# Kernel optimization log

Measured on AMD Instinct MI355X. Metric: run time of the kernel, lower is better.

## Reference

```python
import jax, jax.numpy as jnp
import numpy as np

NUM_ROI = 400
N_GRAPHS = 128
N_NODES = NUM_ROI * N_GRAPHS            # 51200
N_EDGES = N_NODES * 40                  # 2048000
EMB = [128, 128]
BN_EPS = 1e-5


def mish(x):
    return x * jnp.tanh(jax.nn.softplus(x))


def gcn_conv(x, row, col, ew, W, b, n_nodes):
    """PyG GCNConv: h = XW; add self-loops (w=1); sym-normalize; scatter-add; + bias."""
    h = x @ W                                            # [N, out]
    loops = jnp.arange(n_nodes, dtype=row.dtype)
    row_ = jnp.concatenate([row, loops])
    col_ = jnp.concatenate([col, loops])
    ew_ = jnp.concatenate([ew, jnp.ones((n_nodes,), ew.dtype)])
    deg = jax.ops.segment_sum(ew_, col_, num_segments=n_nodes)
    dinv = jnp.where(deg > 0, jax.lax.rsqrt(deg), 0.0)
    norm = dinv[row_] * ew_ * dinv[col_]                 # [E+N]
    msg = norm[:, None] * h[row_]                        # gather + scale
    out = jax.ops.segment_sum(msg, col_, num_segments=n_nodes)
    return out + b


def setup_inputs() -> dict:
    key = jax.random.key(0)
    ks = jax.random.split(key, 16)
    inp = {
        "x": jax.random.normal(ks[0], (N_NODES, NUM_ROI), jnp.float32),
        "edge_index": jax.random.randint(ks[1], (2, N_EDGES), 0, N_NODES, jnp.int64)
        if jax.config.jax_enable_x64 else jax.random.randint(ks[1], (2, N_EDGES), 0, N_NODES, jnp.int32),
        "edge_attr": jax.random.uniform(ks[2], (N_EDGES,), jnp.float32),
        "batch": jnp.repeat(jnp.arange(N_GRAPHS), NUM_ROI),
        "conv1_w": jax.random.normal(ks[3], (NUM_ROI, EMB[0]), jnp.float32) * 0.05,
        "conv1_b": jax.random.normal(ks[4], (EMB[0],), jnp.float32) * 0.05,
        "conv2_w": jax.random.normal(ks[5], (EMB[0], EMB[1]), jnp.float32) * 0.05,
        "conv2_b": jax.random.normal(ks[6], (EMB[1],), jnp.float32) * 0.05,
        "ro_w": jax.random.normal(ks[7], (EMB[1], 8), jnp.float32) * 0.05,
        "ro_b": jax.random.normal(ks[8], (8,), jnp.float32) * 0.05,
        "fc1_w": jax.random.normal(ks[9], (8 * NUM_ROI, NUM_ROI), jnp.float32) * 0.02,
        "fc1_b": jax.random.normal(ks[10], (NUM_ROI,), jnp.float32) * 0.02,
        "bn_gamma": jnp.ones((NUM_ROI,), jnp.float32),
        "bn_beta": jnp.zeros((NUM_ROI,), jnp.float32),
        "fc2_w": jax.random.normal(ks[11], (NUM_ROI, 2), jnp.float32) * 0.05,
        "fc2_b": jax.random.normal(ks[12], (2,), jnp.float32) * 0.05,
    }
    return inp


def reference(x, edge_index, edge_attr, batch,
              conv1_w, conv1_b, conv2_w, conv2_b,
              ro_w, ro_b, fc1_w, fc1_b, bn_gamma, bn_beta, fc2_w, fc2_b):
    n = x.shape[0]
    row, col = edge_index[0], edge_index[1]
    h = mish(gcn_conv(x, row, col, edge_attr, conv1_w, conv1_b, n))
    h = mish(gcn_conv(h, row, col, edge_attr, conv2_w, conv2_b, n))
    out = mish(h @ ro_w + ro_b)                          # [N, 8]
    feats = out.reshape(-1, NUM_ROI * 8)                 # [B, 3200]
    z = feats @ fc1_w + fc1_b                            # [B, 400]
    # BatchNorm1d (training mode: batch statistics, biased variance)
    mu = jnp.mean(z, axis=0)
    var = jnp.mean((z - mu) ** 2, axis=0)
    zn = (z - mu) * jax.lax.rsqrt(var + BN_EPS) * bn_gamma + bn_beta
    logits = mish(zn) @ fc2_w + fc2_b                    # [B, 2]
    return logits
```

## Files before the change

### kernel.cpp

```cpp
#include <hip/hip_runtime.h>
#include <hip/hip_fp16.h>
#include <math.h>

#define NN 51200
#define NE 2048000
#define F 128
#define NB 1000
#define EPB 2048
#define NBKT 200

typedef _Float16 half8 __attribute__((ext_vector_type(8)));
typedef float floatx4 __attribute__((ext_vector_type(4)));

__device__ __forceinline__ float mish_f(float x) {
  if (x > 20.0f) return x;
  float e = __expf(x);
  float w = 1.0f + e;
  w = w * w;
  return x * (w - 1.0f) / (w + 1.0f);
}

__global__ __launch_bounds__(256) void k_chist(const int* __restrict__ ei, unsigned* __restrict__ G) {
  __shared__ unsigned hist[NBKT];
  int blk = blockIdx.x, t = threadIdx.x;
  for (int i = t; i < NBKT; i += 256) hist[i] = 0u;
  __syncthreads();
  int base = blk * EPB;
  for (int it = 0; it < EPB; it += 256) {
    int dst = ei[NE + base + it + t];
    atomicAdd(&hist[dst >> 8], 1u);
  }
  __syncthreads();
  for (int i = t; i < NBKT; i += 256) G[(size_t)i * NB + blk] = hist[i];
}

__global__ __launch_bounds__(64) void k_bscan(unsigned* __restrict__ G, unsigned* __restrict__ btot) {
  int b = blockIdx.x, l = threadIdx.x;
  unsigned base = (unsigned)l * 16;
  unsigned loc[16];
  unsigned s = 0;
#pragma unroll
  for (int i = 0; i < 16; ++i) {
    unsigned idx = base + i;
    unsigned x = (idx < NB) ? G[(size_t)b * NB + idx] : 0u;
    loc[i] = s;
    s += x;
  }
  unsigned run = s;
#pragma unroll
  for (int off = 1; off < 64; off <<= 1) {
    unsigned y = __shfl_up(run, off);
    if (l >= off) run += y;
  }
  unsigned excl = run - s;
#pragma unroll
  for (int i = 0; i < 16; ++i) {
    unsigned idx = base + i;
    if (idx < NB) G[(size_t)b * NB + idx] = excl + loc[i];
  }
  if (l == 63) btot[b] = run;
}

__global__ __launch_bounds__(256) void k_bbase(const unsigned* __restrict__ btot, unsigned* __restrict__ bbase) {
  int t = threadIdx.x, lane = t & 63, wid = t >> 6;
  unsigned v = (t < NBKT) ? btot[t] : 0u;
  unsigned x = v;
#pragma unroll
  for (int off = 1; off < 64; off <<= 1) {
    unsigned y = __shfl_up(x, off);
    if (lane >= off) x += y;
  }
  __shared__ unsigned ws4[4];
  if (lane == 63) ws4[wid] = x;
  __syncthreads();
  unsigned woff = 0;
  for (int k = 0; k < wid; ++k) woff += ws4[k];
  if (t < NBKT) bbase[t] = woff + x - v;
  if (t == 255) bbase[NBKT] = woff + x;
}

__global__ __launch_bounds__(256) void k_cscat(const int* __restrict__ ei, const float* __restrict__ ew,
                                               const unsigned* __restrict__ G,
                                               const unsigned* __restrict__ bbase,
                                               uint2* __restrict__ E) {
  __shared__ unsigned cur[NBKT];
  int blk = blockIdx.x, t = threadIdx.x;
  for (int i = t; i < NBKT; i += 256) cur[i] = bbase[i] + G[(size_t)i * NB + blk];
  __syncthreads();
  int base = blk * EPB;
  for (int it = 0; it < EPB; it += 256) {
    int e = base + it + t;
    int dst = ei[NE + e];
    int src = ei[e];
    float w = ew[e];
    unsigned pos = atomicAdd(&cur[dst >> 8], 1u);
    E[pos] = make_uint2((unsigned)src | ((unsigned)(dst & 255) << 16), __float_as_uint(w));
  }
}

__global__ __launch_bounds__(256) void k_fcnt(const uint2* __restrict__ E, const unsigned* __restrict__ bbase,
                                              int* __restrict__ cnt, float* __restrict__ dinv) {
  __shared__ unsigned lc[256];
  __shared__ float ld[256];
  int b = blockIdx.x, t = threadIdx.x;
  lc[t] = 0u;
  ld[t] = 0.f;
  __syncthreads();
  unsigned e0 = bbase[b], e1 = bbase[b + 1];
  for (unsigned e = e0 + t; e < e1; e += 256) {
    uint2 v = E[e];
    unsigned node = (v.x >> 16) & 255u;
    atomicAdd(&lc[node], 1u);
    atomicAdd(&ld[node], __uint_as_float(v.y));
  }
  __syncthreads();
  cnt[b * 256 + t] = (int)lc[t];
  dinv[b * 256 + t] = rsqrtf(ld[t] + 1.0f);
}

__global__ __launch_bounds__(256) void k_scan1(const int* __restrict__ cnt, int* __restrict__ bsum) {
  int i = blockIdx.x * 256 + threadIdx.x;
  int s = cnt[i];
#pragma unroll
  for (int off = 1; off < 64; off <<= 1) s += __shfl_xor(s, off);
  __shared__ int wsum[4];
  if ((threadIdx.x & 63) == 0) wsum[threadIdx.x >> 6] = s;
  __syncthreads();
  if (threadIdx.x == 0) bsum[blockIdx.x] = wsum[0] + wsum[1] + wsum[2] + wsum[3];
}

__global__ __launch_bounds__(256) void k_scan2(const int* __restrict__ bsum, int* __restrict__ boff,
                                               int* __restrict__ rowptr) {
  int t = threadIdx.x;
  int lane = t & 63, wid = t >> 6;
  int v = (t < 200) ? bsum[t] : 0;
  int x = v;
#pragma unroll
  for (int off = 1; off < 64; off <<= 1) {
    int y = __shfl_up(x, off);
    if (lane >= off) x += y;
  }
  __shared__ int ws4[4];
  if (lane == 63) ws4[wid] = x;
  __syncthreads();
  int woff = 0;
  for (int k = 0; k < wid; ++k) woff += ws4[k];
  if (t < 200) boff[t] = woff + x - v;
  if (t == 255) rowptr[NN] = woff + x;
}

__global__ __launch_bounds__(256) void k_scan3(const int* __restrict__ cnt, const int* __restrict__ boff,
                                               int* __restrict__ rowptr) {
  int i = blockIdx.x * 256 + threadIdx.x;
  int t = threadIdx.x;
  int lane = t & 63, wid = t >> 6;
  int v = cnt[i];
  int x = v;
#pragma unroll
  for (int off = 1; off < 64; off <<= 1) {
    int y = __shfl_up(x, off);
    if (lane >= off) x += y;
  }
  __shared__ int ws4[4];
  if (lane == 63) ws4[wid] = x;
  __syncthreads();
  int woff = boff[blockIdx.x];
  for (int k = 0; k < wid; ++k) woff += ws4[k];
  rowptr[i] = woff + x - v;
}

__global__ __launch_bounds__(256) void k_fscat(const uint2* __restrict__ E, const unsigned* __restrict__ bbase,
                                               const int* __restrict__ rowptr, const float* __restrict__ dinv,
                                               int2* __restrict__ csr) {
  __shared__ int cur[256];
  int b = blockIdx.x, t = threadIdx.x;
  cur[t] = rowptr[b * 256 + t];
  __syncthreads();
  unsigned e0 = bbase[b], e1 = bbase[b + 1];
  for (unsigned e = e0 + t; e < e1; e += 256) {
    uint2 v = E[e];
    unsigned node = (v.x >> 16) & 255u;
    int src = (int)(v.x & 0xFFFFu);
    float w = dinv[src] * __uint_as_float(v.y);
    int p = atomicAdd(&cur[node], 1);
    csr[p] = make_int2(src, __float_as_int(w));
  }
}

__global__ void k_prep_w(const float* __restrict__ W, _Float16* __restrict__ Wt, int K) {
  int idx = blockIdx.x * blockDim.x + threadIdx.x;
  if (idx < K * 128) {
    int k = idx >> 7, n = idx & 127;
    Wt[n * K + k] = (_Float16)W[idx];
  }
}

template <bool A_IS_F32>
__global__ __launch_bounds__(256) void k_gemm16(const void* __restrict__ Av,
                                                const _Float16* __restrict__ Wt,
                                                __half* __restrict__ C, int K) {
  __shared__ _Float16 As[128][40];
  __shared__ _Float16 Bs[128][40];
  int t = threadIdx.x;
  int bm = blockIdx.x * 128;
  int w = t >> 6, l = t & 63, rr = l & 15, q = l >> 4;
  int si = t >> 1, sj = (t & 1) * 16;

  floatx4 acc[2][8];
#pragma unroll
  for (int a = 0; a < 2; ++a)
#pragma unroll
    for (int b = 0; b < 8; ++b) acc[a][b] = (floatx4){0.f, 0.f, 0.f, 0.f};

  for (int k0 = 0; k0 < K; k0 += 32) {
    if (A_IS_F32) {
      const float* A = (const float*)Av;
      half8 h0, h1;
      if (k0 + sj < K) {
        const float* ap = A + (size_t)(bm + si) * K + k0 + sj;
        float4 v0 = *(const float4*)(ap + 0);
        float4 v1 = *(const float4*)(ap + 4);
        float4 v2 = *(const float4*)(ap + 8);
        float4 v3 = *(const float4*)(ap + 12);
        h0 = (half8){(_Float16)v0.x, (_Float16)v0.y, (_Float16)v0.z, (_Float16)v0.w,
                     (_Float16)v1.x, (_Float16)v1.y, (_Float16)v1.z, (_Float16)v1.w};
        h1 = (half8){(_Float16)v2.x, (_Float16)v2.y, (_Float16)v2.z, (_Float16)v2.w,
                     (_Float16)v3.x, (_Float16)v3.y, (_Float16)v3.z, (_Float16)v3.w};
      } else {
        h0 = (half8){0, 0, 0, 0, 0, 0, 0, 0};
        h1 = h0;
      }
      *(half8*)&As[si][sj] = h0;
      *(half8*)&As[si][sj + 8] = h1;
    } else {
      const __half* A = (const __half*)Av;
      uint4 u0, u1;
      if (k0 + sj < K) {
        const __half* ap = A + (size_t)(bm + si) * K + k0 + sj;
        u0 = *(const uint4*)ap;
        u1 = *(const uint4*)(ap + 8);
      } else {
        u0 = make_uint4(0, 0, 0, 0);
        u1 = u0;
      }
      *(uint4*)&As[si][sj] = u0;
      *(uint4*)&As[si][sj + 8] = u1;
    }
    {
      uint4 u0, u1;
      if (k0 + sj < K) {
        const _Float16* wp = Wt + (size_t)si * K + k0 + sj;
        u0 = *(const uint4*)wp;
        u1 = *(const uint4*)(wp + 8);
      } else {
        u0 = make_uint4(0, 0, 0, 0);
        u1 = u0;
      }
      *(uint4*)&Bs[si][sj] = u0;
      *(uint4*)&Bs[si][sj + 8] = u1;
    }
    __syncthreads();

    half8 a0 = *(const half8*)&As[w * 32 + rr][q * 8];
    half8 a1 = *(const half8*)&As[w * 32 + 16 + rr][q * 8];
#pragma unroll
    for (int nt = 0; nt < 8; ++nt) {
      half8 b = *(const half8*)&Bs[nt * 16 + rr][q * 8];
      acc[0][nt] = __builtin_amdgcn_mfma_f32_16x16x32_f16(a0, b, acc[0][nt], 0, 0, 0);
      acc[1][nt] = __builtin_amdgcn_mfma_f32_16x16x32_f16(a1, b, acc[1][nt], 0, 0, 0);
    }
    __syncthreads();
  }
#pragma unroll
  for (int mt = 0; mt < 2; ++mt)
#pragma unroll
    for (int nt = 0; nt < 8; ++nt)
#pragma unroll
      for (int r4 = 0; r4 < 4; ++r4) {
        int row = bm + w * 32 + mt * 16 + q * 4 + r4;
        C[(size_t)row * 128 + nt * 16 + rr] = __float2half(acc[mt][nt][r4]);
      }
}

__global__ __launch_bounds__(256) void k_agg(const __half2* __restrict__ h, const int* __restrict__ rowptr,
                                             const int2* __restrict__ csr, const float* __restrict__ dinv,
                                             const float* __restrict__ bias, __half2* __restrict__ out) {
  unsigned lane = threadIdx.x & 63u;
  int n = blockIdx.x * 4 + (threadIdx.x >> 6);
  float di = dinv[n];
  float2 self = __half22float2(h[((unsigned)n << 6) + lane]);
  float sx = 0.f, sy = 0.f;
  int p = __builtin_amdgcn_readfirstlane(rowptr[n]);
  int p1 = __builtin_amdgcn_readfirstlane(rowptr[n + 1]);
  for (; p + 16 <= p1; p += 16) {
    int2 c[16];
#pragma unroll
    for (int u = 0; u < 16; ++u) c[u] = csr[p + u];
    float2 f[16];
#pragma unroll
    for (int u = 0; u < 16; ++u) f[u] = __half22float2(h[((unsigned)c[u].x << 6) + lane]);
#pragma unroll
    for (int u = 0; u < 16; ++u) {
      float w = __int_as_float(c[u].y);
      sx += w * f[u].x;
      sy += w * f[u].y;
    }
  }
  for (; p + 4 <= p1; p += 4) {
    int2 c[4];
#pragma unroll
    for (int u = 0; u < 4; ++u) c[u] = csr[p + u];
    float2 f[4];
#pragma unroll
    for (int u = 0; u < 4; ++u) f[u] = __half22float2(h[((unsigned)c[u].x << 6) + lane]);
#pragma unroll
    for (int u = 0; u < 4; ++u) {
      float w = __int_as_float(c[u].y);
      sx += w * f[u].x;
      sy += w * f[u].y;
    }
  }
  for (; p < p1; ++p) {
    int2 c0 = csr[p];
    float2 f0 = __half22float2(h[((unsigned)c0.x << 6) + lane]);
    float w = __int_as_float(c0.y);
    sx += w * f0.x;
    sy += w * f0.y;
  }
  float ax = di * (di * self.x + sx);
  float ay = di * (di * self.y + sy);
  float2 bb = ((const float2*)bias)[lane];
  out[((unsigned)n << 6) + lane] = __floats2half2_rn(mish_f(ax + bb.x), mish_f(ay + bb.y));
}

__global__ __launch_bounds__(256) void k_ro(const __half2* __restrict__ h, const float* __restrict__ rw,
                                            const float* __restrict__ rb, float* __restrict__ o8) {
  __shared__ float w[128 * 8];
  int t = threadIdx.x;
  for (int i = t; i < 1024; i += 256) w[i] = rw[i];
  __syncthreads();
  int n = blockIdx.x * 32 + (t >> 3);
  int k = t & 7;
  const __half2* hr = h + (size_t)n * 64;
  float acc = rb[k];
#pragma unroll 4
  for (int j = 0; j < 64; ++j) {
    float2 hv = __half22float2(hr[j]);
    acc += hv.x * w[(2 * j) * 8 + k] + hv.y * w[(2 * j + 1) * 8 + k];
  }
  o8[(size_t)n * 8 + k] = mish_f(acc);
}

__global__ void k_fc1_init(const float* __restrict__ b, float* __restrict__ z) {
  int i = blockIdx.x * blockDim.x + threadIdx.x;
  if (i < 128 * 400) z[i] = b[i % 400];
}

__global__ __launch_bounds__(448) void k_fc1(const float* __restrict__ feats, const float* __restrict__ w,
                                             float* __restrict__ z) {
  __shared__ float fs[8][128];
  int t = threadIdx.x;
  int kc = blockIdx.x * 128;
  int g0 = blockIdx.y * 8;
  for (int i = t; i < 1024; i += 448) {
    int g = i >> 7, k = i & 127;
    fs[g][k] = feats[(size_t)(g0 + g) * 3200 + kc + k];
  }
  __syncthreads();
  if (t < 400) {
    float a[8];
#pragma unroll
    for (int g = 0; g < 8; ++g) a[g] = 0.0f;
    for (int k = 0; k < 128; ++k) {
      float wv = w[(size_t)(kc + k) * 400 + t];
#pragma unroll
      for (int g = 0; g < 8; ++g) a[g] += fs[g][k] * wv;
    }
#pragma unroll
    for (int g = 0; g < 8; ++g) atomicAdd(&z[(size_t)(g0 + g) * 400 + t], a[g]);
  }
}

__global__ __launch_bounds__(128) void k_bn(const float* __restrict__ z, const float* __restrict__ gamma,
                                            const float* __restrict__ beta, float* __restrict__ gs,
                                            float* __restrict__ gb) {
  int j = blockIdx.x;
  int b = threadIdx.x;
  float v = z[b * 400 + j];
  float s = v, s2 = v * v;
#pragma unroll
  for (int off = 1; off < 64; off <<= 1) {
    s += __shfl_xor(s, off);
    s2 += __shfl_xor(s2, off);
  }
  __shared__ float ls[2], ls2[2];
  if ((b & 63) == 0) {
    ls[b >> 6] = s;
    ls2[b >> 6] = s2;
  }
  __syncthreads();
  if (b == 0) {
    float mu = (ls[0] + ls[1]) * (1.0f / 128.0f);
    float var = (ls2[0] + ls2[1]) * (1.0f / 128.0f) - mu * mu;
    float rs = rsqrtf(var + 1e-5f);
    float g = gamma[j] * rs;
    gs[j] = g;
    gb[j] = beta[j] - mu * g;
  }
}

__global__ __launch_bounds__(256) void k_fc2(const float* __restrict__ z, const float* __restrict__ gs,
                                             const float* __restrict__ gb, const float* __restrict__ w2,
                                             const float* __restrict__ b2, float* __restrict__ out) {
  int bg = blockIdx.x;
  int t = threadIdx.x;
  float a0 = 0.f, a1 = 0.f;
  for (int j = t; j < 400; j += 256) {
    float zn = z[bg * 400 + j] * gs[j] + gb[j];
    float m = mish_f(zn);
    a0 += m * w2[j * 2];
    a1 += m * w2[j * 2 + 1];
  }
#pragma unroll
  for (int off = 1; off < 64; off <<= 1) {
    a0 += __shfl_xor(a0, off);
    a1 += __shfl_xor(a1, off);
  }
  __shared__ float s0[4], s1[4];
  if ((t & 63) == 0) {
    s0[t >> 6] = a0;
    s1[t >> 6] = a1;
  }
  __syncthreads();
  if (t == 0) {
    out[bg * 2 + 0] = b2[0] + s0[0] + s0[1] + s0[2] + s0[3];
    out[bg * 2 + 1] = b2[1] + s1[0] + s1[1] + s1[2] + s1[3];
  }
}

extern "C" void kernel_launch(void* const* d_in, const int* in_sizes, int n_in,
                              void* d_out, int out_size, void* d_ws, size_t ws_size,
                              hipStream_t stream) {
  (void)in_sizes; (void)n_in; (void)out_size; (void)ws_size;
  const float* x   = (const float*)d_in[0];
  const int*   ei  = (const int*)d_in[1];
  const float* ew  = (const float*)d_in[2];
  const float* c1w = (const float*)d_in[4];
  const float* c1b = (const float*)d_in[5];
  const float* c2w = (const float*)d_in[6];
  const float* c2b = (const float*)d_in[7];
  const float* rw  = (const float*)d_in[8];
  const float* rb  = (const float*)d_in[9];
  const float* f1w = (const float*)d_in[10];
  const float* f1b = (const float*)d_in[11];
  const float* bng = (const float*)d_in[12];
  const float* bnb = (const float*)d_in[13];
  const float* f2w = (const float*)d_in[14];
  const float* f2b = (const float*)d_in[15];
  float* out = (float*)d_out;

  char* ws = (char*)d_ws;
  size_t off = 0;
  auto alloc = [&](size_t bytes) {
    void* p = ws + off;
    off = (off + bytes + 255) & ~(size_t)255;
    return p;
  };
  float* dinv    = (float*)alloc((size_t)NN * 4);
  int*   cnt     = (int*)alloc((size_t)NN * 4);
  int*   rowptr  = (int*)alloc((size_t)(NN + 1) * 4);
  int*   bsum    = (int*)alloc(200 * 4);
  int*   boff    = (int*)alloc(200 * 4);
  unsigned* G    = (unsigned*)alloc((size_t)NBKT * NB * 4);
  unsigned* btot = (unsigned*)alloc(NBKT * 4);
  unsigned* bbase= (unsigned*)alloc((NBKT + 1) * 4);
  int2*  csr     = (int2*)alloc((size_t)NE * 8);
  __half* A1     = (__half*)alloc((size_t)NN * F * 2);
  __half* B1     = (__half*)alloc((size_t)NN * F * 2);
  _Float16* Wt1  = (_Float16*)alloc((size_t)400 * 128 * 2);
  _Float16* Wt2  = (_Float16*)alloc((size_t)128 * 128 * 2);
  float* o8      = (float*)alloc((size_t)NN * 8 * 4);
  float* z       = (float*)alloc((size_t)128 * 400 * 4);
  float* gs      = (float*)alloc(400 * 4);
  float* gb      = (float*)alloc(400 * 4);

  uint2* E = (uint2*)A1;

  k_chist<<<NB, 256, 0, stream>>>(ei, G);
  k_bscan<<<NBKT, 64, 0, stream>>>(G, btot);
  k_bbase<<<1, 256, 0, stream>>>(btot, bbase);
  k_cscat<<<NB, 256, 0, stream>>>(ei, ew, G, bbase, E);
  k_fcnt<<<NBKT, 256, 0, stream>>>(E, bbase, cnt, dinv);
  k_scan1<<<NN / 256, 256, 0, stream>>>(cnt, bsum);
  k_scan2<<<1, 256, 0, stream>>>(bsum, boff, rowptr);
  k_scan3<<<NN / 256, 256, 0, stream>>>(cnt, boff, rowptr);
  k_fscat<<<NBKT, 256, 0, stream>>>(E, bbase, rowptr, dinv, csr);

  k_prep_w<<<(400 * 128 + 255) / 256, 256, 0, stream>>>(c1w, Wt1, 400);
  k_prep_w<<<(128 * 128 + 255) / 256, 256, 0, stream>>>(c2w, Wt2, 128);

  k_gemm16<true><<<NN / 128, 256, 0, stream>>>(x, Wt1, A1, 400);
  k_agg<<<NN / 4, 256, 0, stream>>>((const __half2*)A1, rowptr, csr, dinv, c1b, (__half2*)B1);
  k_gemm16<false><<<NN / 128, 256, 0, stream>>>(B1, Wt2, A1, 128);
  k_agg<<<NN / 4, 256, 0, stream>>>((const __half2*)A1, rowptr, csr, dinv, c2b, (__half2*)B1);
  k_ro<<<NN / 32, 256, 0, stream>>>((const __half2*)B1, rw, rb, o8);
  k_fc1_init<<<(128 * 400 + 255) / 256, 256, 0, stream>>>(f1b, z);
  {
    dim3 g(25, 16);
    k_fc1<<<g, 448, 0, stream>>>(o8, f1w, z);
  }
  k_bn<<<400, 128, 0, stream>>>(z, bng, bnb, gs, gb);
  k_fc2<<<128, 256, 0, stream>>>(z, gs, gb, f2w, f2b, out);
}
```

Baseline: 438.8 us.

## Pack CSR entries into 32-bit src+fp16 weight and merge init kernels

CSR entries shrink from int2 (src, fp32 weight) to a single 32-bit word holding a 16-bit source index and an fp16 normalized weight, written with nontemporal stores. This halves the CSR bytes the two aggregation kernels read. The two weight-prep kernels and the z init are folded into one k_init launch. z is now zero-initialized instead of bias-initialized, which relies on fc1's bias cancelling under batch-norm mean subtraction. The 16-bit source index assumes edge sources fall within each 65536-node bucket encoding, and fp16 weights cost some precision.

```diff
diff --git a/kernel.cpp b/kernel.cpp
--- a/kernel.cpp
+++ b/kernel.cpp
@@ -18,6 +18,21 @@
   float w = 1.0f + e;
   w = w * w;
   return x * (w - 1.0f) / (w + 1.0f);
+}
+
+__global__ __launch_bounds__(256) void k_init(const float* __restrict__ W1, const float* __restrict__ W2,
+                                              _Float16* __restrict__ Wt1, _Float16* __restrict__ Wt2,
+                                              float* __restrict__ z) {
+  int idx = blockIdx.x * 256 + threadIdx.x;
+  if (idx < 51200) {
+    int k = idx >> 7, n = idx & 127;
+    Wt1[n * 400 + k] = (_Float16)W1[idx];
+    z[idx] = 0.0f;
+  } else {
+    int i2 = idx - 51200;
+    int k = i2 >> 7, n = i2 & 127;
+    Wt2[n * 128 + k] = (_Float16)W2[i2];
+  }
 }
 
 __global__ __launch_bounds__(256) void k_chist(const int* __restrict__ ei, unsigned* __restrict__ G) {
@@ -171,7 +186,7 @@
 
 __global__ __launch_bounds__(256) void k_fscat(const uint2* __restrict__ E, const unsigned* __restrict__ bbase,
                                                const int* __restrict__ rowptr, const float* __restrict__ dinv,
-                                               int2* __restrict__ csr) {
+                                               unsigned* __restrict__ csr) {
   __shared__ int cur[256];
   int b = blockIdx.x, t = threadIdx.x;
   cur[t] = rowptr[b * 256 + t];
@@ -180,18 +195,11 @@
   for (unsigned e = e0 + t; e < e1; e += 256) {
     uint2 v = E[e];
     unsigned node = (v.x >> 16) & 255u;
-    int src = (int)(v.x & 0xFFFFu);
+    unsigned src = v.x & 0xFFFFu;
     float w = dinv[src] * __uint_as_float(v.y);
     int p = atomicAdd(&cur[node], 1);
-    csr[p] = make_int2(src, __float_as_int(w));
-  }
-}
-
-__global__ void k_prep_w(const float* __restrict__ W, _Float16* __restrict__ Wt, int K) {
-  int idx = blockIdx.x * blockDim.x + threadIdx.x;
-  if (idx < K * 128) {
-    int k = idx >> 7, n = idx & 127;
-    Wt[n * K + k] = (_Float16)W[idx];
+    unsigned pk = src | ((unsigned)__half_as_ushort(__float2half_rn(w)) << 16);
+    __builtin_nontemporal_store(pk, &csr[p]);
   }
 }
 
@@ -283,7 +291,7 @@
 }
 
 __global__ __launch_bounds__(256) void k_agg(const __half2* __restrict__ h, const int* __restrict__ rowptr,
-                                             const int2* __restrict__ csr, const float* __restrict__ dinv,
+                                             const unsigned* __restrict__ csr, const float* __restrict__ dinv,
                                              const float* __restrict__ bias, __half2* __restrict__ out) {
   unsigned lane = threadIdx.x & 63u;
   int n = blockIdx.x * 4 + (threadIdx.x >> 6);
@@ -293,37 +301,37 @@
   int p = __builtin_amdgcn_readfirstlane(rowptr[n]);
   int p1 = __builtin_amdgcn_readfirstlane(rowptr[n + 1]);
   for (; p + 16 <= p1; p += 16) {
-    int2 c[16];
+    unsigned c[16];
 #pragma unroll
     for (int u = 0; u < 16; ++u) c[u] = csr[p + u];
     float2 f[16];
 #pragma unroll
-    for (int u = 0; u < 16; ++u) f[u] = __half22float2(h[((unsigned)c[u].x << 6) + lane]);
+    for (int u = 0; u < 16; ++u) f[u] = __half22float2(h[((c[u] & 0xFFFFu) << 6) + lane]);
 #pragma unroll
     for (int u = 0; u < 16; ++u) {
-      float w = __int_as_float(c[u].y);
+      float w = __half2float(__ushort_as_half((unsigned short)(c[u] >> 16)));
       sx += w * f[u].x;
       sy += w * f[u].y;
     }
   }
   for (; p + 4 <= p1; p += 4) {
-    int2 c[4];
+    unsigned c[4];
 #pragma unroll
     for (int u = 0; u < 4; ++u) c[u] = csr[p + u];
     float2 f[4];
 #pragma unroll
-    for (int u = 0; u < 4; ++u) f[u] = __half22float2(h[((unsigned)c[u].x << 6) + lane]);
+    for (int u = 0; u < 4; ++u) f[u] = __half22float2(h[((c[u] & 0xFFFFu) << 6) + lane]);
 #pragma unroll
     for (int u = 0; u < 4; ++u) {
-      float w = __int_as_float(c[u].y);
+      float w = __half2float(__ushort_as_half((unsigned short)(c[u] >> 16)));
       sx += w * f[u].x;
       sy += w * f[u].y;
     }
   }
   for (; p < p1; ++p) {
-    int2 c0 = csr[p];
-    float2 f0 = __half22float2(h[((unsigned)c0.x << 6) + lane]);
-    float w = __int_as_float(c0.y);
+    unsigned c0 = csr[p];
+    float2 f0 = __half22float2(h[((c0 & 0xFFFFu) << 6) + lane]);
+    float w = __half2float(__ushort_as_half((unsigned short)(c0 >> 16)));
     sx += w * f0.x;
     sy += w * f0.y;
   }
@@ -349,11 +357,6 @@
     acc += hv.x * w[(2 * j) * 8 + k] + hv.y * w[(2 * j + 1) * 8 + k];
   }
   o8[(size_t)n * 8 + k] = mish_f(acc);
-}
-
-__global__ void k_fc1_init(const float* __restrict__ b, float* __restrict__ z) {
-  int i = blockIdx.x * blockDim.x + threadIdx.x;
-  if (i < 128 * 400) z[i] = b[i % 400];
 }
 
 __global__ __launch_bounds__(448) void k_fc1(const float* __restrict__ feats, const float* __restrict__ w,
@@ -452,7 +455,6 @@
   const float* rw  = (const float*)d_in[8];
   const float* rb  = (const float*)d_in[9];
   const float* f1w = (const float*)d_in[10];
-  const float* f1b = (const float*)d_in[11];
   const float* bng = (const float*)d_in[12];
   const float* bnb = (const float*)d_in[13];
   const float* f2w = (const float*)d_in[14];
@@ -474,7 +476,7 @@
   unsigned* G    = (unsigned*)alloc((size_t)NBKT * NB * 4);
   unsigned* btot = (unsigned*)alloc(NBKT * 4);
   unsigned* bbase= (unsigned*)alloc((NBKT + 1) * 4);
-  int2*  csr     = (int2*)alloc((size_t)NE * 8);
+  unsigned* csr  = (unsigned*)alloc((size_t)NE * 4 + 64);
   __half* A1     = (__half*)alloc((size_t)NN * F * 2);
   __half* B1     = (__half*)alloc((size_t)NN * F * 2);
   _Float16* Wt1  = (_Float16*)alloc((size_t)400 * 128 * 2);
@@ -486,6 +488,7 @@
 
   uint2* E = (uint2*)A1;
 
+  k_init<<<264, 256, 0, stream>>>(c1w, c2w, Wt1, Wt2, z);
   k_chist<<<NB, 256, 0, stream>>>(ei, G);
   k_bscan<<<NBKT, 64, 0, stream>>>(G, btot);
   k_bbase<<<1, 256, 0, stream>>>(btot, bbase);
@@ -496,15 +499,11 @@
   k_scan3<<<NN / 256, 256, 0, stream>>>(cnt, boff, rowptr);
   k_fscat<<<NBKT, 256, 0, stream>>>(E, bbase, rowptr, dinv, csr);
 
-  k_prep_w<<<(400 * 128 + 255) / 256, 256, 0, stream>>>(c1w, Wt1, 400);
-  k_prep_w<<<(128 * 128 + 255) / 256, 256, 0, stream>>>(c2w, Wt2, 128);
-
   k_gemm16<true><<<NN / 128, 256, 0, stream>>>(x, Wt1, A1, 400);
   k_agg<<<NN / 4, 256, 0, stream>>>((const __half2*)A1, rowptr, csr, dinv, c1b, (__half2*)B1);
   k_gemm16<false><<<NN / 128, 256, 0, stream>>>(B1, Wt2, A1, 128);
   k_agg<<<NN / 4, 256, 0, stream>>>((const __half2*)A1, rowptr, csr, dinv, c2b, (__half2*)B1);
   k_ro<<<NN / 32, 256, 0, stream>>>((const __half2*)B1, rw, rb, o8);
-  k_fc1_init<<<(128 * 400 + 255) / 256, 256, 0, stream>>>(f1b, z);
   {
     dim3 g(25, 16);
     k_fc1<<<g, 448, 0, stream>>>(o8, f1w, z);
```

Result: slower. 472.8 us (+7.7%).
